# Kernel optimization log

Hardware: AMD Instinct MI355X
Metric: run time of the kernel (lower is better)

The kernel has to match this reference:

```python
import jax, jax.numpy as jnp
import numpy as np

EPS = 1e-12  # torch F.normalize eps

def _normalize(v):
    return v / jnp.maximum(jnp.linalg.norm(v, axis=-1, keepdims=True), EPS)

def setup_inputs() -> dict:
    key = jax.random.key(0)
    ks = jax.random.split(key, 8)
    N, K, D = 500000, 32, 3
    positions = jax.random.normal(ks[0], (N, D), dtype=jnp.float32)
    neighbors = jax.random.normal(ks[1], (N, K, D), dtype=jnp.float32)
    # tiny MLP params: Linear(D,5) -> ReLU -> Linear(5,5) -> ReLU -> Linear(5,1)
    s1 = 1.0 / np.sqrt(D)
    s2 = 1.0 / np.sqrt(5)
    W1 = jax.random.uniform(ks[2], (5, D), jnp.float32, -s1, s1)
    b1 = jax.random.uniform(ks[3], (5,), jnp.float32, -s1, s1)
    W2 = jax.random.uniform(ks[4], (5, 5), jnp.float32, -s2, s2)
    b2 = jax.random.uniform(ks[5], (5,), jnp.float32, -s2, s2)
    W3 = jax.random.uniform(ks[6], (1, 5), jnp.float32, -s2, s2)
    b3 = jax.random.uniform(ks[7], (1,), jnp.float32, -s2, s2)
    return {"positions": positions, "neighbors": neighbors,
            "W1": W1, "b1": b1, "W2": W2, "b2": b2, "W3": W3, "b3": b3}

def reference(positions, neighbors, W1, b1, W2, b2, W3, b3):
    # [N,K,D] normalized neighbor difference vectors
    diffs = neighbors - positions[:, None, :]
    nd = _normalize(diffs)
    # tiny MLP producing a scalar weight per neighbor
    h = jax.nn.relu(jnp.einsum('nkd,hd->nkh', nd, W1) + b1)
    h = jax.nn.relu(jnp.einsum('nkh,gh->nkg', h, W2) + b2)
    w = jnp.einsum('nkh,oh->nko', h, W3) + b3  # [N,K,1]
    vel = jnp.sum(nd * w, axis=1)  # [N,D]
    return _normalize(vel)
```

## Files before the change

### kernel.cpp

```cpp
#include <hip/hip_runtime.h>


#define K 32

__global__ __launch_bounds__(256) void velvec_kernel(
    const float* __restrict__ pos,
    const float* __restrict__ nbr,
    const float* __restrict__ W1,
    const float* __restrict__ b1,
    const float* __restrict__ W2,
    const float* __restrict__ b2,
    const float* __restrict__ W3,
    const float* __restrict__ b3,
    float* __restrict__ out,
    int N)
{
    const int lane  = threadIdx.x & (K - 1);
    const int point = (int)((blockIdx.x * blockDim.x + threadIdx.x) >> 5);
    if (point >= N) return;

    float w1[5][3], bb1[5], w2[5][5], bb2[5], w3[5];
#pragma unroll
    for (int h = 0; h < 5; ++h) {
        bb1[h] = b1[h];
        bb2[h] = b2[h];
        w3[h]  = W3[h];
#pragma unroll
        for (int d = 0; d < 3; ++d) w1[h][d] = W1[h * 3 + d];
#pragma unroll
        for (int g = 0; g < 5; ++g) w2[h][g] = W2[h * 5 + g];
    }
    const float bb3 = b3[0];

    const float px = pos[point * 3 + 0];
    const float py = pos[point * 3 + 1];
    const float pz = pos[point * 3 + 2];

    const float* nb = nbr + (size_t)point * (K * 3) + lane * 3;
    float dx = nb[0] - px;
    float dy = nb[1] - py;
    float dz = nb[2] - pz;
    float n2 = dx * dx + dy * dy + dz * dz;
    float inv = (n2 > 1e-24f) ? __builtin_amdgcn_rsqf(n2) : 1e12f;
    dx *= inv; dy *= inv; dz *= inv;

    float h1[5];
#pragma unroll
    for (int h = 0; h < 5; ++h) {
        float a = bb1[h];
        a = fmaf(w1[h][0], dx, a);
        a = fmaf(w1[h][1], dy, a);
        a = fmaf(w1[h][2], dz, a);
        h1[h] = fmaxf(a, 0.0f);
    }
    float h2[5];
#pragma unroll
    for (int g = 0; g < 5; ++g) {
        float a = bb2[g];
#pragma unroll
        for (int h = 0; h < 5; ++h) a = fmaf(w2[g][h], h1[h], a);
        h2[g] = fmaxf(a, 0.0f);
    }
    float w = bb3;
#pragma unroll
    for (int h = 0; h < 5; ++h) w = fmaf(w3[h], h2[h], w);

    float vx = dx * w, vy = dy * w, vz = dz * w;
#pragma unroll
    for (int m = 16; m > 0; m >>= 1) {
        vx += __shfl_xor(vx, m, K);
        vy += __shfl_xor(vy, m, K);
        vz += __shfl_xor(vz, m, K);
    }

    float vn2  = vx * vx + vy * vy + vz * vz;
    float vinv = (vn2 > 1e-24f) ? __builtin_amdgcn_rsqf(vn2) : 1e12f;
    if (lane < 3) {
        float c = (lane == 0) ? vx : (lane == 1) ? vy : vz;
        out[point * 3 + lane] = c * vinv;
    }
}

extern "C" void kernel_launch(void* const* d_in, const int* in_sizes, int n_in,
                              void* d_out, int out_size, void* d_ws, size_t ws_size,
                              hipStream_t stream) {
    const float* pos = (const float*)d_in[0];
    const float* nbr = (const float*)d_in[1];
    const float* W1  = (const float*)d_in[2];
    const float* b1  = (const float*)d_in[3];
    const float* W2  = (const float*)d_in[4];
    const float* b2  = (const float*)d_in[5];
    const float* W3  = (const float*)d_in[6];
    const float* b3  = (const float*)d_in[7];
    float* out = (float*)d_out;

    const int N = in_sizes[0] / 3;
    const int threads = 256;
    const long long total = (long long)N * K;
    const int blocks = (int)((total + threads - 1) / threads);

    velvec_kernel<<<blocks, threads, 0, stream>>>(pos, nbr, W1, b1, W2, b2, W3, b3,
                                                  out, N);
}
```

Baseline: 279.7 us.

## Map one thread per point and loop over neighbors with vector loads

Switches from 32 lanes per point with a shuffle reduction to a single thread per point that processes all 32 neighbors sequentially using float4 loads. This removes the cross-lane shuffle reduction, the redundant per-lane weight and position loads, and the partial-lane output writes. In exchange, global accesses become strided across threads rather than coalesced, and the grid has far fewer threads, which lowers latency hiding.

```diff
diff --git a/kernel.cpp b/kernel.cpp
--- a/kernel.cpp
+++ b/kernel.cpp
@@ -15,8 +15,7 @@
     float* __restrict__ out,
     int N)
 {
-    const int lane  = threadIdx.x & (K - 1);
-    const int point = (int)((blockIdx.x * blockDim.x + threadIdx.x) >> 5);
+    const int point = blockIdx.x * blockDim.x + threadIdx.x;
     if (point >= N) return;
 
     float w1[5][3], bb1[5], w2[5][5], bb2[5], w3[5];
@@ -36,49 +35,62 @@
     const float py = pos[point * 3 + 1];
     const float pz = pos[point * 3 + 2];
 
-    const float* nb = nbr + (size_t)point * (K * 3) + lane * 3;
-    float dx = nb[0] - px;
-    float dy = nb[1] - py;
-    float dz = nb[2] - pz;
-    float n2 = dx * dx + dy * dy + dz * dz;
-    float inv = (n2 > 1e-24f) ? __builtin_amdgcn_rsqf(n2) : 1e12f;
-    dx *= inv; dy *= inv; dz *= inv;
+    const float4* nb4 = (const float4*)(nbr + (size_t)point * (K * 3));
 
-    float h1[5];
+    float vx = 0.0f, vy = 0.0f, vz = 0.0f;
+
 #pragma unroll
-    for (int h = 0; h < 5; ++h) {
-        float a = bb1[h];
-        a = fmaf(w1[h][0], dx, a);
-        a = fmaf(w1[h][1], dy, a);
-        a = fmaf(w1[h][2], dz, a);
-        h1[h] = fmaxf(a, 0.0f);
-    }
-    float h2[5];
+    for (int c = 0; c < 8; ++c) {
+        const float4 f0 = nb4[c * 3 + 0];
+        const float4 f1 = nb4[c * 3 + 1];
+        const float4 f2 = nb4[c * 3 + 2];
+        float nx[4], ny[4], nz[4];
+        nx[0] = f0.x; ny[0] = f0.y; nz[0] = f0.z;
+        nx[1] = f0.w; ny[1] = f1.x; nz[1] = f1.y;
+        nx[2] = f1.z; ny[2] = f1.w; nz[2] = f2.x;
+        nx[3] = f2.y; ny[3] = f2.z; nz[3] = f2.w;
+
 #pragma unroll
-    for (int g = 0; g < 5; ++g) {
-        float a = bb2[g];
+        for (int j = 0; j < 4; ++j) {
+            float dx = nx[j] - px;
+            float dy = ny[j] - py;
+            float dz = nz[j] - pz;
+            float n2 = dx * dx + dy * dy + dz * dz;
+            float inv = (n2 > 1e-24f) ? __builtin_amdgcn_rsqf(n2) : 1e12f;
+            dx *= inv; dy *= inv; dz *= inv;
+
+            float h1[5];
 #pragma unroll
-        for (int h = 0; h < 5; ++h) a = fmaf(w2[g][h], h1[h], a);
-        h2[g] = fmaxf(a, 0.0f);
-    }
-    float w = bb3;
+            for (int h = 0; h < 5; ++h) {
+                float a = bb1[h];
+                a = fmaf(w1[h][0], dx, a);
+                a = fmaf(w1[h][1], dy, a);
+                a = fmaf(w1[h][2], dz, a);
+                h1[h] = fmaxf(a, 0.0f);
+            }
+            float h2[5];
 #pragma unroll
-    for (int h = 0; h < 5; ++h) w = fmaf(w3[h], h2[h], w);
+            for (int g = 0; g < 5; ++g) {
+                float a = bb2[g];
+#pragma unroll
+                for (int h = 0; h < 5; ++h) a = fmaf(w2[g][h], h1[h], a);
+                h2[g] = fmaxf(a, 0.0f);
+            }
+            float w = bb3;
+#pragma unroll
+            for (int h = 0; h < 5; ++h) w = fmaf(w3[h], h2[h], w);
 
-    float vx = dx * w, vy = dy * w, vz = dz * w;
-#pragma unroll
-    for (int m = 16; m > 0; m >>= 1) {
-        vx += __shfl_xor(vx, m, K);
-        vy += __shfl_xor(vy, m, K);
-        vz += __shfl_xor(vz, m, K);
+            vx = fmaf(dx, w, vx);
+            vy = fmaf(dy, w, vy);
+            vz = fmaf(dz, w, vz);
+        }
     }
 
     float vn2  = vx * vx + vy * vy + vz * vz;
     float vinv = (vn2 > 1e-24f) ? __builtin_amdgcn_rsqf(vn2) : 1e12f;
-    if (lane < 3) {
-        float c = (lane == 0) ? vx : (lane == 1) ? vy : vz;
-        out[point * 3 + lane] = c * vinv;
-    }
+    out[point * 3 + 0] = vx * vinv;
+    out[point * 3 + 1] = vy * vinv;
+    out[point * 3 + 2] = vz * vinv;
 }
 
 extern "C" void kernel_launch(void* const* d_in, const int* in_sizes, int n_in,
@@ -96,8 +108,7 @@
 
     const int N = in_sizes[0] / 3;
     const int threads = 256;
-    const long long total = (long long)N * K;
-    const int blocks = (int)((total + threads - 1) / threads);
+    const int blocks = (N + threads - 1) / threads;
 
     velvec_kernel<<<blocks, threads, 0, stream>>>(pos, nbr, W1, b1, W2, b2, W3, b3,
                                                   out, N);
```

Result: slower. 294.5 us (+5.3%).
